# Kernel tuning notes

Hardware: AMD Instinct MI355X
Metric: run time of the kernel (lower is better)

## Reference

```python
import jax, jax.numpy as jnp
import numpy as np

G, S, M = 4, 2048, 1024   # groups (batch), tokens per group, emb dim
E, H, K = 8, 4096, 2      # experts, mlp dim, top-k
CAP = int(K * S / E * 1.25)  # expert capacity = 640
AUX_COEF, Z_COEF = 0.01, 0.001


def setup_inputs() -> dict:
    key = jax.random.key(0)
    k1, k2, k3, k4, k5 = jax.random.split(key, 5)
    return {
        "inputs": jax.random.normal(k1, (G, S, M), jnp.float32),
        "paddings": jnp.zeros((G, S), jnp.float32),  # 1.0 = padded token
        "router_w": jax.random.normal(k2, (M, E), jnp.float32) / np.sqrt(M),
        "wi_gate": jax.random.normal(k3, (E, M, H), jnp.float32) / np.sqrt(M),
        "wi_0": jax.random.normal(k4, (E, M, H), jnp.float32) / np.sqrt(M),
        "wo": jax.random.normal(k5, (E, H, M), jnp.float32) / np.sqrt(H),
    }


def reference(inputs, paddings, router_w, wi_gate, wi_0, wo):
    # Router
    logits = jnp.einsum('gsm,me->gse', inputs, router_w)          # [G,S,E]
    probs = jax.nn.softmax(logits, axis=-1)
    top_p, top_i = jax.lax.top_k(probs, K)                        # [G,S,K]

    nonpad = 1.0 - paddings                                       # [G,S]
    exp_mask = jax.nn.one_hot(top_i, E, dtype=jnp.float32)        # [G,S,K,E]
    exp_mask = exp_mask * nonpad[:, :, None, None]

    # Position in expert (capacity-limited), priority by token order then k slot
    mask_flat = exp_mask.reshape(G, S * K, E)
    pos = jnp.cumsum(mask_flat, axis=1) * mask_flat               # 1-indexed where assigned
    keep = mask_flat * (pos <= CAP)
    pos_oh = jax.nn.one_hot((pos - 1.0).astype(jnp.int32), CAP, dtype=jnp.float32)  # [G,SK,E,CAP]
    dispatch_k = (keep[..., None] * pos_oh).reshape(G, S, K, E, CAP)
    dispatch = dispatch_k.sum(axis=2)                             # [G,S,E,CAP]
    combine = jnp.einsum('gsk,gskec->gsec', top_p, dispatch_k)    # [G,S,E,CAP]

    # Dispatch -> gated expert FFN -> combine
    expert_in = jnp.einsum('gsec,gsm->egcm', dispatch, inputs)    # [E,G,CAP,M]
    h = jax.nn.silu(jnp.einsum('egcm,emh->egch', expert_in, wi_gate)) \
        * jnp.einsum('egcm,emh->egch', expert_in, wi_0)           # [E,G,CAP,H]
    expert_out = jnp.einsum('egch,ehm->egcm', h, wo)              # [E,G,CAP,M]
    output = jnp.einsum('gsec,egcm->gsm', combine, expert_out)    # [G,S,M]

    # Aux losses: load-balancing (Switch style) + router z-loss
    em = jnp.max(jax.nn.one_hot(top_i, E, dtype=jnp.float32), axis=-2)       # [G,S,E]
    lb = jnp.mean(jnp.mean(em, axis=-2) * jnp.mean(probs, axis=-2)) * E * E
    z = jnp.mean(jax.nn.logsumexp(logits, axis=-1) ** 2)
    aux_loss = AUX_COEF * lb + Z_COEF * z
    return output, aux_loss
```

## Files before the change

kernel.cpp:

```cpp
#include <hip/hip_runtime.h>
#include <hip/hip_bf16.h>
#include <math.h>

#define G 4
#define S 2048
#define MDIM 1024
#define E 8
#define HDIM 4096
#define TOPK 2
#define CAP 640
#define GC (G*CAP)
#define RBLK (G*S/4)

typedef __attribute__((ext_vector_type(8))) short bf16x8;
typedef __attribute__((ext_vector_type(4))) short s16x4;
typedef __attribute__((ext_vector_type(4))) float f32x4;
typedef __attribute__((ext_vector_type(16))) float f32x16;
typedef unsigned int u32;
typedef unsigned short u16;

#define MFMA32(a,b,c) __builtin_amdgcn_mfma_f32_32x32x16_bf16(a,b,c,0,0,0)
#define BAR() __builtin_amdgcn_s_barrier()

__device__ __forceinline__ u16 f2bf(float f) {
    union { float f; u32 u; } v; v.f = f;
    u32 r = v.u + 0x7fffu + ((v.u >> 16) & 1u);
    return (u16)(r >> 16);
}

__device__ __forceinline__ void gload16(const char* gp, char* lp) {
    __builtin_amdgcn_global_load_lds((const __attribute__((address_space(1))) u32*)gp,
                                     (__attribute__((address_space(3))) u32*)lp,
                                     16, 0, 0);
}

__device__ __forceinline__ int swz128(int r) { return ((r >> 1) & 7) << 4; }

__device__ void transpose_body(const float* __restrict__ in, u16* __restrict__ out,
                               int R, int C, int tb, float (*tile)[68]) {
    int nbx = C / 64, nby = R / 64;
    int bx = tb % nbx, by = (tb / nbx) % nby, e = tb / (nbx * nby);
    const float* ine = in + (size_t)e * R * C;
    u16* oute = out + (size_t)e * R * C;
    int t = threadIdx.x;
    int x0 = bx * 64, y0 = by * 64;
    int lx = (t & 15) * 4, ly = t >> 4;
    #pragma unroll
    for (int i = 0; i < 4; ++i) {
        f32x4 v = *(const f32x4*)(ine + (size_t)(y0 + ly + i * 16) * C + x0 + lx);
        *(f32x4*)&tile[ly + i * 16][lx] = v;
    }
    __syncthreads();
    int rr0 = (t & 15) * 4, cb = t >> 4;
    #pragma unroll
    for (int p = 0; p < 4; ++p) {
        int cc = cb + p * 16;
        s16x4 pk;
        #pragma unroll
        for (int j = 0; j < 4; ++j) pk[j] = (short)f2bf(tile[rr0 + j][cc]);
        *(s16x4*)(oute + (size_t)(x0 + cc) * R + y0 + rr0) = pk;
    }
}

__global__ __launch_bounds__(256) void prep_kernel(
        const float* __restrict__ inp, const float* __restrict__ rw,
        const float* __restrict__ wi_gate, const float* __restrict__ wi_0,
        const float* __restrict__ wo,
        u16* __restrict__ WgT, u16* __restrict__ W0T, u16* __restrict__ WoT,
        int* __restrict__ top_i, float* __restrict__ top_p,
        float* __restrict__ partials) {
    __shared__ float tile[64][68];
    __shared__ float part[4][17];
    int bid = blockIdx.x;
    if (bid >= RBLK) {
        int tb = bid - RBLK;
        if (tb < 8192)       transpose_body(wi_gate, WgT, MDIM, HDIM, tb, tile);
        else if (tb < 16384) transpose_body(wi_0,   W0T, MDIM, HDIM, tb - 8192, tile);
        else                 transpose_body(wo,     WoT, HDIM, MDIM, tb - 16384, tile);
        return;
    }
    int wid = threadIdx.x >> 6, lane = threadIdx.x & 63;
    int tok = bid * 4 + wid;
    const float* x = inp + (size_t)tok * MDIM;
    float acc[E] = {0.f,0.f,0.f,0.f,0.f,0.f,0.f,0.f};
    #pragma unroll
    for (int rep = 0; rep < 4; ++rep) {
        int m0 = rep * 256 + lane * 4;
        f32x4 xv = *(const f32x4*)(x + m0);
        #pragma unroll
        for (int j = 0; j < 4; ++j) {
            const float* r = rw + (size_t)(m0 + j) * E;
            float xj = xv[j];
            #pragma unroll
            for (int e = 0; e < E; ++e) acc[e] += xj * r[e];
        }
    }
    #pragma unroll
    for (int e = 0; e < E; ++e)
        #pragma unroll
        for (int off = 32; off; off >>= 1) acc[e] += __shfl_down(acc[e], off);

    if (lane == 0) {
        float mx = acc[0];
        #pragma unroll
        for (int e = 1; e < E; ++e) mx = fmaxf(mx, acc[e]);
        float p[E], sum = 0.f;
        #pragma unroll
        for (int e = 0; e < E; ++e) { p[e] = expf(acc[e] - mx); sum += p[e]; }
        float inv = 1.f / sum;
        #pragma unroll
        for (int e = 0; e < E; ++e) p[e] *= inv;
        float lse = logf(sum) + mx;
        int i0 = 0;
        #pragma unroll
        for (int e = 1; e < E; ++e) if (acc[e] > acc[i0]) i0 = e;
        int i1 = (i0 == 0) ? 1 : 0;
        #pragma unroll
        for (int e = 0; e < E; ++e) if (e != i0 && acc[e] > acc[i1]) i1 = e;
        top_i[tok*2+0] = i0; top_i[tok*2+1] = i1;
        top_p[tok*2+0] = p[i0]; top_p[tok*2+1] = p[i1];
        #pragma unroll
        for (int e = 0; e < E; ++e) { part[wid][e] = p[e]; part[wid][8+e] = 0.f; }
        part[wid][8+i0] = 1.f; part[wid][8+i1] = 1.f;
        part[wid][16] = lse * lse;
    }
    __syncthreads();
    if (threadIdx.x < 17) {
        float v = part[0][threadIdx.x] + part[1][threadIdx.x] +
                  part[2][threadIdx.x] + part[3][threadIdx.x];
        partials[(size_t)bid * 17 + threadIdx.x] = v;
    }
}

__global__ __launch_bounds__(256) void scan_reduce_kernel(
        const int* __restrict__ top_i, const float* __restrict__ pad,
        const float* __restrict__ partials,
        int* __restrict__ slot_token, int* __restrict__ token_c,
        float* __restrict__ sums_out) {
    __shared__ int sums[256];
    __shared__ float red[256];
    int bid = blockIdx.x;
    int t = threadIdx.x;
    if (bid >= 32) {
        int g = bid - 32;
        float loc[17];
        #pragma unroll
        for (int c = 0; c < 17; ++c) loc[c] = 0.f;
        for (int r = t; r < 512; r += 256) {
            const float* pr = partials + ((size_t)g * 512 + r) * 17;
            #pragma unroll
            for (int c = 0; c < 17; ++c) loc[c] += pr[c];
        }
        for (int c = 0; c < 17; ++c) {
            red[t] = loc[c]; __syncthreads();
            for (int off = 128; off; off >>= 1) {
                if (t < off) red[t] += red[t + off];
                __syncthreads();
            }
            if (t == 0) sums_out[g * 17 + c] = red[0];
            __syncthreads();
        }
        return;
    }
    int g = bid >> 3, e = bid & 7;
    int base = t * 16;
    int run = 0; unsigned mask16 = 0; int loc[16];
    #pragma unroll
    for (int j = 0; j < 16; ++j) {
        int i = base + j; int s = i >> 1, k = i & 1;
        int ex = top_i[((size_t)(g * S + s)) * 2 + k];
        int m = (ex == e) && (pad[g * S + s] == 0.f);
        run += m; loc[j] = run; mask16 |= ((unsigned)m << j);
    }
    sums[t] = run; __syncthreads();
    for (int off = 1; off < 256; off <<= 1) {
        int v = (t >= off) ? sums[t - off] : 0;
        __syncthreads();
        sums[t] += v;
        __syncthreads();
    }
    int excl = sums[t] - run;
    #pragma unroll
    for (int j = 0; j < 16; ++j) {
        if ((mask16 >> j) & 1u) {
            int pos = excl + loc[j];
            if (pos <= CAP) {
                int i = base + j; int s = i >> 1, k = i & 1;
                slot_token[((size_t)(e * G + g)) * CAP + (pos - 1)] = s;
                token_c[((size_t)(g * S + s)) * 2 + k] = pos - 1;
            }
        }
    }
}

__global__ __launch_bounds__(128) void gather_kernel(const float* __restrict__ inp,
                                                     const int* __restrict__ slot_token,
                                                     u16* __restrict__ X) {
    int row = blockIdx.x;
    int t = threadIdx.x;
    int s = slot_token[row];
    int g = (row % GC) / CAP;
    bf16x8 v;
    if (s >= 0) {
        const float* src = inp + ((size_t)(g * S + s)) * MDIM + t * 8;
        f32x4 a = *(const f32x4*)src;
        f32x4 b = *(const f32x4*)(src + 4);
        #pragma unroll
        for (int j = 0; j < 4; ++j) { v[j] = (short)f2bf(a[j]); v[4+j] = (short)f2bf(b[j]); }
    } else {
        #pragma unroll
        for (int j = 0; j < 8; ++j) v[j] = 0;
    }
    *(bf16x8*)(X + (size_t)row * MDIM + t * 8) = v;
}

__global__ __launch_bounds__(512, 1) void gemm_ffn12_v9(
        const u16* __restrict__ Xb, const u16* __restrict__ WgT,
        const u16* __restrict__ W0T, u16* __restrict__ Hb) {
    extern __shared__ char smem[];
    const int NK = MDIM / 64;
    int bid = blockIdx.x;
    int swz = (bid & 7) * 320 + (bid >> 3);
    int mt = swz % 10, nt = (swz / 10) & 31, e = swz / 320;
    const char* A  = (const char*)(Xb  + (size_t)e * GC * MDIM   + (size_t)mt * 256 * MDIM);
    const char* Bg = (const char*)(WgT + (size_t)e * HDIM * MDIM + (size_t)nt * 128 * MDIM);
    const char* B0 = (const char*)(W0T + (size_t)e * HDIM * MDIM + (size_t)nt * 128 * MDIM);
    int tid = threadIdx.x, w = tid >> 6, l = tid & 63;
    int wm = w >> 2, wn = w & 3;
    int lr = l & 31, lk = l >> 5;
    int lswz = ((lr >> 1) & 7) << 4;

    int koff[4];
    #pragma unroll
    for (int ks = 0; ks < 4; ++ks) koff[ks] = (ks * 32 + lk * 16) ^ lswz;
    int baseA[4];
    #pragma unroll
    for (int rb = 0; rb < 4; ++rb) baseA[rb] = (wm * 128 + rb * 32 + lr) * 128;
    int baseB = (wn * 32 + lr) * 128;

    const char* srcA[4]; const char* srcG[2]; const char* srcO[2];
    #pragma unroll
    for (int p = 0; p < 4; ++p) {
        int gr = p * 64 + w * 8 + (l >> 3);
        srcA[p] = A + (size_t)gr * (MDIM * 2) + (((l & 7) * 16) ^ swz128(gr));
    }
    #pragma unroll
    for (int p = 0; p < 2; ++p) {
        int gr = p * 64 + w * 8 + (l >> 3);
        srcG[p] = Bg + (size_t)gr * (MDIM * 2) + (((l & 7) * 16) ^ swz128(gr));
        srcO[p] = B0 + (size_t)gr * (MDIM * 2) + (((l & 7) * 16) ^ swz128(gr));
    }

    f32x16 zz;
    #pragma unroll
    for (int i = 0; i < 16; ++i) zz[i] = 0.f;
    f32x16 ag[4], ao[4];
    #pragma unroll
    for (int rb = 0; rb < 4; ++rb) { ag[rb] = zz; ao[rb] = zz; }

    auto stage = [&](int tt) {
        int kk = tt * 128;
        char* dst = smem + (tt & 1) * 65536;
        #pragma unroll
        for (int p = 0; p < 4; ++p)
            gload16(srcA[p] + kk, dst + (p * 64 + w * 8) * 128);
        #pragma unroll
        for (int p = 0; p < 2; ++p) {
            gload16(srcG[p] + kk, dst + 32768 + (p * 64 + w * 8) * 128);
            gload16(srcO[p] + kk, dst + 49152 + (p * 64 + w * 8) * 128);
        }
    };

    stage(0);
    asm volatile("s_waitcnt vmcnt(0)" ::: "memory");
    BAR();

    #pragma unroll 1
    for (int t = 0; t < NK; ++t) {
        if (t + 1 < NK) stage(t + 1);
        const char* bufc = smem + (t & 1) * 65536;
        #pragma unroll
        for (int ks = 0; ks < 4; ++ks) {
            bf16x8 bg = *(const bf16x8*)(bufc + 32768 + baseB + koff[ks]);
            bf16x8 bo = *(const bf16x8*)(bufc + 49152 + baseB + koff[ks]);
            bf16x8 af[4];
            #pragma unroll
            for (int rb = 0; rb < 4; ++rb)
                af[rb] = *(const bf16x8*)(bufc + baseA[rb] + koff[ks]);
            __builtin_amdgcn_s_setprio(1);
            #pragma unroll
            for (int rb = 0; rb < 4; ++rb) {
                ag[rb] = MFMA32(bg, af[rb], ag[rb]);
                ao[rb] = MFMA32(bo, af[rb], ao[rb]);
            }
            __builtin_amdgcn_s_setprio(0);
        }
        asm volatile("s_waitcnt vmcnt(0)" ::: "memory");
        BAR();
    }

    u16* He = Hb + (size_t)e * GC * HDIM;
    int row0 = mt * 256 + wm * 128 + lr;
    int col0 = nt * 128 + wn * 32 + lk * 4;
    #pragma unroll
    for (int rb = 0; rb < 4; ++rb) {
        size_t rowoff = (size_t)(row0 + rb * 32) * HDIM;
        #pragma unroll
        for (int q = 0; q < 4; ++q) {
            s16x4 pk;
            #pragma unroll
            for (int r = 0; r < 4; ++r) {
                float gv = ag[rb][q * 4 + r], ov = ao[rb][q * 4 + r];
                float hv = gv / (1.f + __expf(-gv)) * ov;
                pk[r] = (short)f2bf(hv);
            }
            *(s16x4*)(He + rowoff + col0 + q * 8) = pk;
        }
    }
}

__global__ __launch_bounds__(512, 1) void gemm_out_v9(
        const u16* __restrict__ Hb, const u16* __restrict__ WoT,
        float* __restrict__ EO) {
    extern __shared__ char smem[];
    const int NK = HDIM / 64;
    int bid = blockIdx.x;
    int swz = (bid & 7) * 80 + (bid >> 3);
    int nt = swz & 3, mt = (swz / 4) % 20, e = swz / 80;
    const char* A = (const char*)(Hb  + (size_t)e * GC * HDIM   + (size_t)mt * 128 * HDIM);
    const char* B = (const char*)(WoT + (size_t)e * MDIM * HDIM + (size_t)nt * 256 * HDIM);
    int tid = threadIdx.x, w = tid >> 6, l = tid & 63;
    int wm = w >> 2, wn = w & 3;
    int lr = l & 31, lk = l >> 5;
    int lswz = ((lr >> 1) & 7) << 4;

    int koff[4];
    #pragma unroll
    for (int ks = 0; ks < 4; ++ks) koff[ks] = (ks * 32 + lk * 16) ^ lswz;
    int baseA[2], baseB[2];
    #pragma unroll
    for (int rb = 0; rb < 2; ++rb) baseA[rb] = (wm * 64 + rb * 32 + lr) * 128;
    #pragma unroll
    for (int cb = 0; cb < 2; ++cb) baseB[cb] = (wn * 64 + cb * 32 + lr) * 128;

    const char* srcA[2]; const char* srcB[4];
    #pragma unroll
    for (int p = 0; p < 2; ++p) {
        int gr = p * 64 + w * 8 + (l >> 3);
        srcA[p] = A + (size_t)gr * (HDIM * 2) + (((l & 7) * 16) ^ swz128(gr));
    }
    #pragma unroll
    for (int p = 0; p < 4; ++p) {
        int gr = p * 64 + w * 8 + (l >> 3);
        srcB[p] = B + (size_t)gr * (HDIM * 2) + (((l & 7) * 16) ^ swz128(gr));
    }

    f32x16 zz;
    #pragma unroll
    for (int i = 0; i < 16; ++i) zz[i] = 0.f;
    f32x16 acc[2][2];
    #pragma unroll
    for (int i = 0; i < 2; ++i)
        #pragma unroll
        for (int j = 0; j < 2; ++j) acc[i][j] = zz;

    auto stage = [&](int tt) {
        int kk = tt * 128;
        char* dst = smem + (tt & 1) * 49152;
        #pragma unroll
        for (int p = 0; p < 2; ++p)
            gload16(srcA[p] + kk, dst + (p * 64 + w * 8) * 128);
        #pragma unroll
        for (int p = 0; p < 4; ++p)
            gload16(srcB[p] + kk, dst + 16384 + (p * 64 + w * 8) * 128);
    };

    stage(0);
    asm volatile("s_waitcnt vmcnt(0)" ::: "memory");
    BAR();

    #pragma unroll 1
    for (int t = 0; t < NK; ++t) {
        if (t + 1 < NK) stage(t + 1);
        const char* bufc = smem + (t & 1) * 49152;
        #pragma unroll
        for (int ks = 0; ks < 4; ++ks) {
            bf16x8 bf[2], af[2];
            #pragma unroll
            for (int cb = 0; cb < 2; ++cb)
                bf[cb] = *(const bf16x8*)(bufc + 16384 + baseB[cb] + koff[ks]);
            #pragma unroll
            for (int rb = 0; rb < 2; ++rb)
                af[rb] = *(const bf16x8*)(bufc + baseA[rb] + koff[ks]);
            __builtin_amdgcn_s_setprio(1);
            #pragma unroll
            for (int rb = 0; rb < 2; ++rb)
                #pragma unroll
                for (int cb = 0; cb < 2; ++cb)
                    acc[rb][cb] = MFMA32(bf[cb], af[rb], acc[rb][cb]);
            __builtin_amdgcn_s_setprio(0);
        }
        asm volatile("s_waitcnt vmcnt(0)" ::: "memory");
        BAR();
    }

    float* Ee = EO + (size_t)e * GC * MDIM;
    int row0 = mt * 128 + wm * 64 + lr;
    int col0 = nt * 256 + wn * 64 + lk * 4;
    #pragma unroll
    for (int rb = 0; rb < 2; ++rb) {
        size_t rowoff = (size_t)(row0 + rb * 32) * MDIM;
        #pragma unroll
        for (int cb = 0; cb < 2; ++cb)
            #pragma unroll
            for (int q = 0; q < 4; ++q) {
                f32x4 v;
                #pragma unroll
                for (int r = 0; r < 4; ++r) v[r] = acc[rb][cb][q * 4 + r];
                *(f32x4*)(Ee + rowoff + col0 + cb * 32 + q * 8) = v;
            }
    }
}

__global__ __launch_bounds__(256) void combine_aux_kernel(
        const float* __restrict__ EO, const int* __restrict__ top_i,
        const float* __restrict__ top_p, const int* __restrict__ token_c,
        const float* __restrict__ sums, float* __restrict__ out) {
    int bid = blockIdx.x;
    if (bid == G * S) {
        if (threadIdx.x == 0) {
            float lb = 0.f, z = 0.f;
            for (int g = 0; g < G; ++g) {
                for (int e = 0; e < E; ++e)
                    lb += (sums[g*17 + 8 + e] / (float)S) * (sums[g*17 + e] / (float)S);
                z += sums[g*17 + 16];
            }
            lb = lb / (float)(G * E) * (float)(E * E);
            z /= (float)(G * S);
            out[(size_t)G * S * MDIM] = 0.01f * lb + 0.001f * z;
        }
        return;
    }
    int tok = bid, t = threadIdx.x;
    int g = tok >> 11;
    f32x4 acc = {0.f, 0.f, 0.f, 0.f};
    #pragma unroll
    for (int k = 0; k < 2; ++k) {
        int c = token_c[tok * 2 + k];
        if (c >= 0) {
            int e = top_i[tok * 2 + k];
            float p = top_p[tok * 2 + k];
            const float* src = EO + ((size_t)e * GC + g * CAP + c) * MDIM + t * 4;
            f32x4 v = *(const f32x4*)src;
            #pragma unroll
            for (int j = 0; j < 4; ++j) acc[j] += p * v[j];
        }
    }
    *(f32x4*)(out + (size_t)tok * MDIM + t * 4) = acc;
}

extern "C" void kernel_launch(void* const* d_in, const int* in_sizes, int n_in,
                              void* d_out, int out_size, void* d_ws, size_t ws_size,
                              hipStream_t stream) {
    (void)in_sizes; (void)n_in; (void)out_size; (void)ws_size;
    const float* inputs   = (const float*)d_in[0];
    const float* paddings = (const float*)d_in[1];
    const float* router_w = (const float*)d_in[2];
    const float* wi_gate  = (const float*)d_in[3];
    const float* wi_0     = (const float*)d_in[4];
    const float* wo       = (const float*)d_in[5];
    float* out = (float*)d_out;

    char* p = (char*)d_ws;
    u16* WgT = (u16*)p; p += (size_t)E * HDIM * MDIM * 2;
    u16* W0T = (u16*)p; p += (size_t)E * HDIM * MDIM * 2;
    u16* WoT = (u16*)p; p += (size_t)E * HDIM * MDIM * 2;
    u16* Xb  = (u16*)p; p += (size_t)E * GC * MDIM * 2;
    u16* Hb  = (u16*)p; p += (size_t)E * GC * HDIM * 2;
    float* EO = (float*)p; p += (size_t)E * GC * MDIM * 4;
    int*   top_i = (int*)p;   p += (size_t)G * S * TOPK * 4;
    float* top_p = (float*)p; p += (size_t)G * S * TOPK * 4;
    int*   token_c = (int*)p; p += (size_t)G * S * TOPK * 4;
    int*   slot_token = (int*)p; p += (size_t)E * G * CAP * 4;
    float* partials = (float*)p; p += (size_t)RBLK * 17 * 4;
    float* sums = (float*)p; p += 4 * 17 * 4;

    hipMemsetAsync(token_c, 0xFF, (size_t)G * S * TOPK * 4, stream);
    hipMemsetAsync(slot_token, 0xFF, (size_t)E * G * CAP * 4, stream);

    hipFuncSetAttribute((const void*)gemm_ffn12_v9,
                        hipFuncAttributeMaxDynamicSharedMemorySize, 131072);
    hipFuncSetAttribute((const void*)gemm_out_v9,
                        hipFuncAttributeMaxDynamicSharedMemorySize, 98304);

    prep_kernel<<<RBLK + 24576, 256, 0, stream>>>(inputs, router_w, wi_gate, wi_0, wo,
                                                  WgT, W0T, WoT, top_i, top_p, partials);
    scan_reduce_kernel<<<36, 256, 0, stream>>>(top_i, paddings, partials,
                                               slot_token, token_c, sums);
    gather_kernel<<<E * GC, 128, 0, stream>>>(inputs, slot_token, Xb);
    gemm_ffn12_v9<<<2560, 512, 131072, stream>>>(Xb, WgT, W0T, Hb);
    gemm_out_v9<<<640, 512, 98304, stream>>>(Hb, WoT, EO);
    combine_aux_kernel<<<G * S + 1, 256, 0, stream>>>(EO, top_i, top_p, token_c,
                                                      sums, out);
}
```

Before: 763.2 us.

## Rewrite gate/up GEMM with 16x16 MFMA and fine-grained split-K LDS pipeline

```diff
diff --git a/kernel.cpp b/kernel.cpp
--- a/kernel.cpp
+++ b/kernel.cpp
@@ -19,8 +19,11 @@
 typedef unsigned int u32;
 typedef unsigned short u16;
 
+#define MFMA16(a,b,c) __builtin_amdgcn_mfma_f32_16x16x32_bf16(a,b,c,0,0,0)
 #define MFMA32(a,b,c) __builtin_amdgcn_mfma_f32_32x32x16_bf16(a,b,c,0,0,0)
 #define BAR() __builtin_amdgcn_s_barrier()
+#define SB0() __builtin_amdgcn_sched_barrier(0)
+#define LGKM0() asm volatile("s_waitcnt lgkmcnt(0)" ::: "memory")
 
 __device__ __forceinline__ u16 f2bf(float f) {
     union { float f; u32 u; } v; v.f = f;
@@ -35,6 +38,7 @@
 }
 
 __device__ __forceinline__ int swz128(int r) { return ((r >> 1) & 7) << 4; }
+__device__ __forceinline__ int swz64(int r)  { return ((r >> 1) & 3) << 4; }
 
 __device__ void transpose_body(const float* __restrict__ in, u16* __restrict__ out,
                                int R, int C, int tb, float (*tile)[68]) {
@@ -214,7 +218,7 @@
     *(bf16x8*)(X + (size_t)row * MDIM + t * 8) = v;
 }
 
-__global__ __launch_bounds__(512, 1) void gemm_ffn12_v9(
+__global__ __launch_bounds__(512, 1) void gemm_ffn12_v11(
         const u16* __restrict__ Xb, const u16* __restrict__ WgT,
         const u16* __restrict__ W0T, u16* __restrict__ Hb) {
     extern __shared__ char smem[];
@@ -227,96 +231,129 @@
     const char* B0 = (const char*)(W0T + (size_t)e * HDIM * MDIM + (size_t)nt * 128 * MDIM);
     int tid = threadIdx.x, w = tid >> 6, l = tid & 63;
     int wm = w >> 2, wn = w & 3;
-    int lr = l & 31, lk = l >> 5;
-    int lswz = ((lr >> 1) & 7) << 4;
-
-    int koff[4];
-    #pragma unroll
-    for (int ks = 0; ks < 4; ++ks) koff[ks] = (ks * 32 + lk * 16) ^ lswz;
-    int baseA[4];
-    #pragma unroll
-    for (int rb = 0; rb < 4; ++rb) baseA[rb] = (wm * 128 + rb * 32 + lr) * 128;
-    int baseB = (wn * 32 + lr) * 128;
-
-    const char* srcA[4]; const char* srcG[2]; const char* srcO[2];
-    #pragma unroll
-    for (int p = 0; p < 4; ++p) {
-        int gr = p * 64 + w * 8 + (l >> 3);
-        srcA[p] = A + (size_t)gr * (MDIM * 2) + (((l & 7) * 16) ^ swz128(gr));
-    }
-    #pragma unroll
-    for (int p = 0; p < 2; ++p) {
-        int gr = p * 64 + w * 8 + (l >> 3);
-        srcG[p] = Bg + (size_t)gr * (MDIM * 2) + (((l & 7) * 16) ^ swz128(gr));
-        srcO[p] = B0 + (size_t)gr * (MDIM * 2) + (((l & 7) * 16) ^ swz128(gr));
-    }
-
-    f32x16 zz;
-    #pragma unroll
-    for (int i = 0; i < 16; ++i) zz[i] = 0.f;
-    f32x16 ag[4], ao[4];
-    #pragma unroll
-    for (int rb = 0; rb < 4; ++rb) { ag[rb] = zz; ao[rb] = zz; }
-
-    auto stage = [&](int tt) {
-        int kk = tt * 128;
-        char* dst = smem + (tt & 1) * 65536;
-        #pragma unroll
-        for (int p = 0; p < 4; ++p)
-            gload16(srcA[p] + kk, dst + (p * 64 + w * 8) * 128);
-        #pragma unroll
-        for (int p = 0; p < 2; ++p) {
-            gload16(srcG[p] + kk, dst + 32768 + (p * 64 + w * 8) * 128);
-            gload16(srcO[p] + kk, dst + 49152 + (p * 64 + w * 8) * 128);
-        }
+    int fr = l & 15, fg = l >> 4;
+
+    int grA0 = (w * 2 + 0) * 16 + (l >> 2), grA1 = (w * 2 + 1) * 16 + (l >> 2);
+    const char* srcA0 = A + (size_t)grA0 * (MDIM * 2) + (((l & 3) * 16) ^ swz64(grA0));
+    const char* srcA1 = A + (size_t)grA1 * (MDIM * 2) + (((l & 3) * 16) ^ swz64(grA1));
+    int grB = w * 16 + (l >> 2);
+    const char* srcG = Bg + (size_t)grB * (MDIM * 2) + (((l & 3) * 16) ^ swz64(grB));
+    const char* srcO = B0 + (size_t)grB * (MDIM * 2) + (((l & 3) * 16) ^ swz64(grB));
+
+    int baseAr[8];
+    #pragma unroll
+    for (int fm = 0; fm < 8; ++fm) {
+        int r = wm * 128 + fm * 16 + fr;
+        baseAr[fm] = r * 64 + ((fg * 16) ^ swz64(r));
+    }
+    int baseGr[2], baseOr[2];
+    #pragma unroll
+    for (int fn = 0; fn < 2; ++fn) {
+        int r = wn * 32 + fn * 16 + fr;
+        baseGr[fn] = 32768 + r * 64 + ((fg * 16) ^ swz64(r));
+        baseOr[fn] = baseGr[fn] + 8192;
+    }
+
+    f32x4 ag[8][2], ao[8][2];
+    #pragma unroll
+    for (int i = 0; i < 8; ++i) {
+        ag[i][0] = (f32x4){0,0,0,0}; ag[i][1] = (f32x4){0,0,0,0};
+        ao[i][0] = (f32x4){0,0,0,0}; ao[i][1] = (f32x4){0,0,0,0};
+    }
+
+    auto stageA = [&](int tt, int ks) {
+        int kk = tt * 128 + ks * 64;
+        char* dst = smem + (tt & 1) * 65536 + ks * 16384;
+        gload16(srcA0 + kk, dst + (w * 2 + 0) * 1024);
+        gload16(srcA1 + kk, dst + (w * 2 + 1) * 1024);
     };
-
-    stage(0);
-    asm volatile("s_waitcnt vmcnt(0)" ::: "memory");
+    auto stageBB = [&](int tt, int ks) {
+        int kk = tt * 128 + ks * 64;
+        char* dst = smem + (tt & 1) * 65536 + 32768 + ks * 16384 + w * 1024;
+        gload16(srcG + kk, dst);
+        gload16(srcO + kk, dst + 8192);
+    };
+
+    stageA(0, 0); stageBB(0, 0); stageA(0, 1); stageBB(0, 1);
+    stageA(1, 0); stageBB(1, 0);
+    asm volatile("s_waitcnt vmcnt(4)" ::: "memory");
     BAR();
+
+    bf16x8 bgf[2], bof[2];
 
     #pragma unroll 1
     for (int t = 0; t < NK; ++t) {
-        if (t + 1 < NK) stage(t + 1);
-        const char* bufc = smem + (t & 1) * 65536;
-        #pragma unroll
-        for (int ks = 0; ks < 4; ++ks) {
-            bf16x8 bg = *(const bf16x8*)(bufc + 32768 + baseB + koff[ks]);
-            bf16x8 bo = *(const bf16x8*)(bufc + 49152 + baseB + koff[ks]);
+        const char* buf = smem + (t & 1) * 65536;
+        #pragma unroll
+        for (int ks = 0; ks < 2; ++ks) {
+            const char* bks = buf + ks * 16384;
             bf16x8 af[4];
-            #pragma unroll
-            for (int rb = 0; rb < 4; ++rb)
-                af[rb] = *(const bf16x8*)(bufc + baseA[rb] + koff[ks]);
+            bgf[0] = *(const bf16x8*)(bks + baseGr[0]);
+            bgf[1] = *(const bf16x8*)(bks + baseGr[1]);
+            bof[0] = *(const bf16x8*)(bks + baseOr[0]);
+            bof[1] = *(const bf16x8*)(bks + baseOr[1]);
+            #pragma unroll
+            for (int j = 0; j < 4; ++j) af[j] = *(const bf16x8*)(bks + baseAr[j]);
+            if (ks == 0) { if (t + 1 < NK) stageA(t + 1, 1); }
+            else         { if (t + 2 < NK) stageA(t + 2, 0); }
+            SB0();
+            BAR();
+            LGKM0(); SB0();
             __builtin_amdgcn_s_setprio(1);
             #pragma unroll
-            for (int rb = 0; rb < 4; ++rb) {
-                ag[rb] = MFMA32(bg, af[rb], ag[rb]);
-                ao[rb] = MFMA32(bo, af[rb], ao[rb]);
+            for (int fm = 0; fm < 4; ++fm)
+                #pragma unroll
+                for (int fn = 0; fn < 2; ++fn) {
+                    ag[fm][fn] = MFMA16(bgf[fn], af[fm], ag[fm][fn]);
+                    ao[fm][fn] = MFMA16(bof[fn], af[fm], ao[fm][fn]);
+                }
+            __builtin_amdgcn_s_setprio(0);
+            BAR();
+            bf16x8 ah[4];
+            #pragma unroll
+            for (int j = 0; j < 4; ++j) ah[j] = *(const bf16x8*)(bks + baseAr[4 + j]);
+            if (ks == 0) { if (t + 1 < NK) stageBB(t + 1, 1); }
+            else         { if (t + 2 < NK) stageBB(t + 2, 0); }
+            SB0();
+            if (ks == 0) {
+                if (t + 1 < NK) { asm volatile("s_waitcnt vmcnt(8)" ::: "memory"); }
+                else            { asm volatile("s_waitcnt vmcnt(0)" ::: "memory"); }
+            } else {
+                if (t + 2 < NK)      { asm volatile("s_waitcnt vmcnt(8)" ::: "memory"); }
+                else if (t + 1 < NK) { asm volatile("s_waitcnt vmcnt(4)" ::: "memory"); }
+                else                 { asm volatile("s_waitcnt vmcnt(0)" ::: "memory"); }
             }
+            BAR();
+            LGKM0(); SB0();
+            __builtin_amdgcn_s_setprio(1);
+            #pragma unroll
+            for (int fm = 0; fm < 4; ++fm)
+                #pragma unroll
+                for (int fn = 0; fn < 2; ++fn) {
+                    ag[4+fm][fn] = MFMA16(bgf[fn], ah[fm], ag[4+fm][fn]);
+                    ao[4+fm][fn] = MFMA16(bof[fn], ah[fm], ao[4+fm][fn]);
+                }
             __builtin_amdgcn_s_setprio(0);
-        }
-        asm volatile("s_waitcnt vmcnt(0)" ::: "memory");
-        BAR();
+            BAR();
+        }
     }
 
     u16* He = Hb + (size_t)e * GC * HDIM;
-    int row0 = mt * 256 + wm * 128 + lr;
-    int col0 = nt * 128 + wn * 32 + lk * 4;
-    #pragma unroll
-    for (int rb = 0; rb < 4; ++rb) {
-        size_t rowoff = (size_t)(row0 + rb * 32) * HDIM;
-        #pragma unroll
-        for (int q = 0; q < 4; ++q) {
+    int row0 = mt * 256 + wm * 128 + fr;
+    int col0 = nt * 128 + wn * 32 + fg * 4;
+    #pragma unroll
+    for (int fm = 0; fm < 8; ++fm)
+        #pragma unroll
+        for (int fn = 0; fn < 2; ++fn) {
             s16x4 pk;
             #pragma unroll
             for (int r = 0; r < 4; ++r) {
-                float gv = ag[rb][q * 4 + r], ov = ao[rb][q * 4 + r];
+                float gv = ag[fm][fn][r], ov = ao[fm][fn][r];
                 float hv = gv / (1.f + __expf(-gv)) * ov;
                 pk[r] = (short)f2bf(hv);
             }
-            *(s16x4*)(He + rowoff + col0 + q * 8) = pk;
-        }
-    }
+            *(s16x4*)(He + (size_t)(row0 + fm * 16) * HDIM + col0 + fn * 16) = pk;
+        }
 }
 
 __global__ __launch_bounds__(512, 1) void gemm_out_v9(
@@ -488,7 +525,7 @@
     hipMemsetAsync(token_c, 0xFF, (size_t)G * S * TOPK * 4, stream);
     hipMemsetAsync(slot_token, 0xFF, (size_t)E * G * CAP * 4, stream);
 
-    hipFuncSetAttribute((const void*)gemm_ffn12_v9,
+    hipFuncSetAttribute((const void*)gemm_ffn12_v11,
                         hipFuncAttributeMaxDynamicSharedMemorySize, 131072);
     hipFuncSetAttribute((const void*)gemm_out_v9,
                         hipFuncAttributeMaxDynamicSharedMemorySize, 98304);
@@ -498,7 +535,7 @@
     scan_reduce_kernel<<<36, 256, 0, stream>>>(top_i, paddings, partials,
                                                slot_token, token_c, sums);
     gather_kernel<<<E * GC, 128, 0, stream>>>(inputs, slot_token, Xb);
-    gemm_ffn12_v9<<<2560, 512, 131072, stream>>>(Xb, WgT, W0T, Hb);
+    gemm_ffn12_v11<<<2560, 512, 131072, stream>>>(Xb, WgT, W0T, Hb);
     gemm_out_v9<<<640, 512, 98304, stream>>>(Hb, WoT, EO);
     combine_aux_kernel<<<G * S + 1, 256, 0, stream>>>(EO, top_i, top_p, token_c,
                                                       sums, out);
```

New measurement: 762.6 us. No clear change (-0.1%).
